# Kernel optimization log

Measured on AMD Instinct MI355X. Metric: run time of the kernel, lower is better.

## Reference

```python
import jax, jax.numpy as jnp
import numpy as np

# Tsit5 Butcher tableau (Tsitouras 2011), same coefficients diffrax uses.
C2, C3, C4, C5, C6 = 0.161, 0.327, 0.9, 0.9800255409045097, 1.0
A21 = 0.161
A31, A32 = -0.008480655492356989, 0.335480655492357
A41, A42, A43 = 2.8971530571054935, -6.359448489975075, 4.3622954328695815
A51, A52, A53, A54 = 5.325864828439257, -11.748883564062828, 7.4955393428898365, -0.09249506636175525
A61, A62, A63, A64, A65 = 5.86145544294642, -12.92096931784711, 8.159367898576159, -0.071584973281401, -0.028269050394068383
B1, B2, B3, B4, B5, B6 = 0.09646076681806523, 0.01, 0.4798896504144996, 1.379008574103742, -3.290069515436081, 2.324710524099774

DIM, WIDTH, DEPTH = 64, 256, 3
BATCH, NT = 4096, 101


def setup_inputs() -> dict:
    key = jax.random.key(0)
    ks = jax.random.split(key, 10)
    ts = jnp.linspace(0.0, 1.0, NT, dtype=jnp.float32)
    y0 = jax.random.normal(ks[0], (BATCH, DIM), dtype=jnp.float32)
    def lin(k, fan_in, fan_out):
        lim = 1.0 / np.sqrt(fan_in)
        kw, kb = jax.random.split(k)
        W = jax.random.uniform(kw, (fan_in, fan_out), jnp.float32, -lim, lim)
        b = jax.random.uniform(kb, (fan_out,), jnp.float32, -lim, lim)
        return W, b
    W0, b0 = lin(ks[1], DIM, WIDTH)
    W1, b1 = lin(ks[2], WIDTH, WIDTH)
    W2, b2 = lin(ks[3], WIDTH, WIDTH)
    W3, b3 = lin(ks[4], WIDTH, DIM)
    return {"ts": ts, "y0": y0, "W0": W0, "b0": b0, "W1": W1, "b1": b1,
            "W2": W2, "b2": b2, "W3": W3, "b3": b3}


def _vf(y, W0, b0, W1, b1, W2, b2, W3, b3):
    # MLP vector field f(t, y) = MLP(y); tanh hidden activations, depth=3 hidden layers.
    h = jnp.tanh(y @ W0 + b0)
    h = jnp.tanh(h @ W1 + b1)
    h = jnp.tanh(h @ W2 + b2)
    return h @ W3 + b3


def reference(ts, y0, W0, b0, W1, b1, W2, b2, W3, b3):
    f = lambda y: _vf(y, W0, b0, W1, b1, W2, b2, W3, b3)

    def tsit5_step(y, h):
        # h: scalar step size (broadcasts over [batch, dim])
        k1 = f(y)
        k2 = f(y + h * (A21 * k1))
        k3 = f(y + h * (A31 * k1 + A32 * k2))
        k4 = f(y + h * (A41 * k1 + A42 * k2 + A43 * k3))
        k5 = f(y + h * (A51 * k1 + A52 * k2 + A53 * k3 + A54 * k4))
        k6 = f(y + h * (A61 * k1 + A62 * k2 + A63 * k3 + A64 * k4 + A65 * k5))
        return y + h * (B1 * k1 + B2 * k2 + B3 * k3 + B4 * k4 + B5 * k5 + B6 * k6)

    def scan_body(y, hpair):
        y_new = tsit5_step(y, hpair)
        return y_new, y_new

    hs = ts[1:] - ts[:-1]                     # [NT-1] step sizes between save points
    hs = hs[:, None, None]                    # broadcast to [NT-1, 1, 1]
    _, ys_tail = jax.lax.scan(scan_body, y0, hs)
    return jnp.concatenate([y0[None], ys_tail], axis=0)  # [NT, batch, dim]
```

## Files before the change

kernel.cpp:

```cpp
#include <hip/hip_runtime.h>

#define NTIME   101
#define BATCH   4096
#define DIM     64
#define WIDTH   256
#define TB      16
#define NTHREADS 1024
#define AST     264
#define SPS     68

#define A21 0.161f
#define A31 (-0.008480655492356989f)
#define A32 0.335480655492357f
#define A41 2.8971530571054935f
#define A42 (-6.359448489975075f)
#define A43 4.3622954328695815f
#define A51 5.325864828439257f
#define A52 (-11.748883564062828f)
#define A53 7.4955393428898365f
#define A54 (-0.09249506636175525f)
#define A61 5.86145544294642f
#define A62 (-12.92096931784711f)
#define A63 8.159367898576159f
#define A64 (-0.071584973281401f)
#define A65 (-0.028269050394068383f)
#define B1 0.09646076681806523f
#define B2 0.01f
#define B3 0.4798896504144996f
#define B4 1.379008574103742f
#define B5 (-3.290069515436081f)
#define B6 2.324710524099774f

typedef float  floatx4 __attribute__((ext_vector_type(4)));
typedef _Float16 halfx8 __attribute__((ext_vector_type(8)));

#define L0S1 0
#define L0S2 16384
#define L1S1 32768
#define L1S2 98304
#define L2S1 163840
#define L2S2 229376
#define L3S1 294912
#define L3S2 311296

__device__ __forceinline__ float fast_tanh(float x) {
    float e = __expf(2.0f * x);
    return 1.0f - 2.0f / (e + 1.0f);
}

__device__ __forceinline__ void bar_lds() {
    asm volatile("s_waitcnt lgkmcnt(0)\n\ts_barrier" ::: "memory");
}

__global__ void pack_weights(const float* __restrict__ W0, const float* __restrict__ W1,
                             const float* __restrict__ W2, const float* __restrict__ W3,
                             _Float16* __restrict__ ws)
{
    int idx = blockIdx.x * 256 + threadIdx.x;
    const float* W; int K, N, e; size_t d1, d2;
    if (idx < 16384)       { W = W0; K = 64;  N = 256; e = idx;          d1 = L0S1; d2 = L0S2; }
    else if (idx < 81920)  { W = W1; K = 256; N = 256; e = idx - 16384;  d1 = L1S1; d2 = L1S2; }
    else if (idx < 147456) { W = W2; K = 256; N = 256; e = idx - 81920;  d1 = L2S1; d2 = L2S2; }
    else if (idx < 163840) { W = W3; K = 256; N = 64;  e = idx - 147456; d1 = L3S1; d2 = L3S2; }
    else return;
    int k = e / N, n = e % N;
    float w = W[e];
    _Float16 h1 = (_Float16)w;
    _Float16 h2 = (_Float16)((w - (float)h1) * 4096.0f);
    int kc = k >> 5, q = (k >> 3) & 3, j = k & 7, nt = n >> 4, nc = n & 15;
    size_t off = ((size_t)((nt * (K / 32) + kc) * 64 + q * 16 + nc)) * 8 + j;
    ws[d1 + off] = h1;
    ws[d2 + off] = h2;
}

template<int KCNT>
__device__ __forceinline__ void mfma_run(const _Float16* __restrict__ pA1,
                                         const _Float16* __restrict__ pA2,
                                         const _Float16* __restrict__ B1g,
                                         const _Float16* __restrict__ B2g,
                                         int fbBase, int kcStart, int lane,
                                         floatx4& acc1o, floatx4& acc2o)
{
    const int m = lane & 15, q = lane >> 4;
    floatx4 acc1 = (floatx4)0.0f, acc2 = (floatx4)0.0f;
    halfx8 va1[2], va2[2], vb1[2], vb2[2];

    const int aOff0 = m * AST + kcStart * 32 + q * 8;
    const size_t fOff0 = ((size_t)fbBase * 64 + lane) * 8;
    vb1[0] = *(const halfx8*)(B1g + fOff0);
    vb2[0] = *(const halfx8*)(B2g + fOff0);
    va1[0] = *(const halfx8*)(pA1 + aOff0);
    va2[0] = *(const halfx8*)(pA2 + aOff0);

    #pragma unroll
    for (int i = 0; i < KCNT; ++i) {
        const int cur = i & 1, nxt = cur ^ 1;
        if (i + 1 < KCNT) {
            const size_t fOff = ((size_t)(fbBase + i + 1) * 64 + lane) * 8;
            vb1[nxt] = *(const halfx8*)(B1g + fOff);
            vb2[nxt] = *(const halfx8*)(B2g + fOff);
            const int aOff = m * AST + (kcStart + i + 1) * 32 + q * 8;
            va1[nxt] = *(const halfx8*)(pA1 + aOff);
            va2[nxt] = *(const halfx8*)(pA2 + aOff);
        }
        acc1 = __builtin_amdgcn_mfma_f32_16x16x32_f16(va1[cur], vb1[cur], acc1, 0, 0, 0);
        acc2 = __builtin_amdgcn_mfma_f32_16x16x32_f16(va1[cur], vb2[cur], acc2, 0, 0, 0);
        acc2 = __builtin_amdgcn_mfma_f32_16x16x32_f16(va2[cur], vb1[cur], acc2, 0, 0, 0);
    }
    acc1o = acc1; acc2o = acc2;
}

__device__ __forceinline__ void hidden_epi(floatx4 a1, floatx4 a2,
                                           const float* __restrict__ bias,
                                           _Float16* __restrict__ o1,
                                           _Float16* __restrict__ o2,
                                           int w, int lane)
{
    const int m = lane & 15, q = lane >> 4;
    const int col = (w << 4) + m;
    const float bb = bias[col];
    #pragma unroll
    for (int v = 0; v < 4; ++v) {
        float val = fast_tanh(a1[v] + a2[v] * (1.0f / 4096.0f) + bb);
        _Float16 h1 = (_Float16)val;
        _Float16 h2 = (_Float16)((val - (float)h1) * 4096.0f);
        const int idx = (q * 4 + v) * AST + col;
        o1[idx] = h1;
        o2[idx] = h2;
    }
}

__global__ void __launch_bounds__(NTHREADS)
ode_kernel(const float* __restrict__ ts, const float* __restrict__ y0,
           const float* __restrict__ b0, const float* __restrict__ b1,
           const float* __restrict__ b2, const float* __restrict__ b3,
           const _Float16* __restrict__ ws, float* __restrict__ out)
{
    __shared__ __align__(16) _Float16 sA1[2][TB * AST];
    __shared__ __align__(16) _Float16 sA2[2][TB * AST];
    __shared__ __align__(16) _Float16 cW0[32768];
    __shared__ __align__(16) float sK[5][TB * DIM];
    __shared__ __align__(16) float sY[TB * DIM];
    __shared__ __align__(16) float sP[4][TB * SPS];
    __shared__ __align__(16) float sBias[832];

    const int tid  = threadIdx.x;
    const int lane = tid & 63;
    const int w    = tid >> 6;
    const long base = (long)blockIdx.x * (TB * DIM);
    const int c = tid & 63;
    const int r = tid >> 6;

    #pragma unroll
    for (int i = 0; i < 4; ++i)
        ((halfx8*)cW0)[tid + i * NTHREADS] = ((const halfx8*)(ws + L0S1))[tid + i * NTHREADS];

    if (tid < 832) {
        float v;
        if (tid < 256)      v = b0[tid];
        else if (tid < 512) v = b1[tid - 256];
        else if (tid < 768) v = b2[tid - 512];
        else                v = b3[tid - 768];
        sBias[tid] = v;
    }
    {
        float v = y0[base + tid];
        sY[tid] = v;
        __builtin_nontemporal_store(v, &out[base + tid]);
        _Float16 h1 = (_Float16)v;
        _Float16 h2 = (_Float16)((v - (float)h1) * 4096.0f);
        sA1[0][r * AST + c] = h1;
        sA2[0][r * AST + c] = h2;
    }
    __syncthreads();

    const int r68 = r * SPS + c;

    for (int t = 0; t < NTIME - 1; ++t) {
        const float h = ts[t + 1] - ts[t];

        #pragma unroll 1
        for (int s = 0; s < 6; ++s) {
            floatx4 a1, a2;
            mfma_run<2>(sA1[0], sA2[0], cW0, cW0 + 16384, w * 2, 0, lane, a1, a2);
            hidden_epi(a1, a2, sBias + 0, sA1[1], sA2[1], w, lane);
            bar_lds();
            mfma_run<8>(sA1[1], sA2[1], ws + L1S1, ws + L1S2, w * 8, 0, lane, a1, a2);
            hidden_epi(a1, a2, sBias + 256, sA1[0], sA2[0], w, lane);
            bar_lds();
            mfma_run<8>(sA1[0], sA2[0], ws + L2S1, ws + L2S2, w * 8, 0, lane, a1, a2);
            hidden_epi(a1, a2, sBias + 512, sA1[1], sA2[1], w, lane);
            bar_lds();
            {
                const int nt = w & 3, kg = w >> 2;
                mfma_run<2>(sA1[1], sA2[1], ws + L3S1, ws + L3S2,
                            nt * 8 + kg * 2, kg * 2, lane, a1, a2);
                const int m = lane & 15, q = lane >> 4;
                #pragma unroll
                for (int v = 0; v < 4; ++v)
                    sP[kg][(q * 4 + v) * SPS + nt * 16 + m]
                        = a1[v] + a2[v] * (1.0f / 4096.0f);
            }
            bar_lds();

            float kv = sP[0][r68] + sP[1][r68] + sP[2][r68] + sP[3][r68]
                     + sBias[768 + c];
            float v;
            if (s == 0) {
                sK[0][tid] = kv;
                v = fmaf(h, A21 * kv, sY[tid]);
            } else if (s == 1) {
                sK[1][tid] = kv;
                v = fmaf(h, fmaf(A31, sK[0][tid], A32 * kv), sY[tid]);
            } else if (s == 2) {
                sK[2][tid] = kv;
                float sum = A41 * sK[0][tid] + A42 * sK[1][tid] + A43 * kv;
                v = fmaf(h, sum, sY[tid]);
            } else if (s == 3) {
                sK[3][tid] = kv;
                float sum = A51 * sK[0][tid] + A52 * sK[1][tid] + A53 * sK[2][tid] + A54 * kv;
                v = fmaf(h, sum, sY[tid]);
            } else if (s == 4) {
                sK[4][tid] = kv;
                float sum = A61 * sK[0][tid] + A62 * sK[1][tid] + A63 * sK[2][tid]
                          + A64 * sK[3][tid] + A65 * kv;
                v = fmaf(h, sum, sY[tid]);
            } else {
                float sum = B1 * sK[0][tid] + B2 * sK[1][tid] + B3 * sK[2][tid]
                          + B4 * sK[3][tid] + B5 * sK[4][tid] + B6 * kv;
                v = fmaf(h, sum, sY[tid]);
                sY[tid] = v;
                __builtin_nontemporal_store(v, &out[(long)(t + 1) * (BATCH * DIM) + base + tid]);
            }
            _Float16 h1 = (_Float16)v;
            _Float16 h2 = (_Float16)((v - (float)h1) * 4096.0f);
            sA1[0][r * AST + c] = h1;
            sA2[0][r * AST + c] = h2;
            bar_lds();
        }
    }
}

extern "C" void kernel_launch(void* const* d_in, const int* in_sizes, int n_in,
                              void* d_out, int out_size, void* d_ws, size_t ws_size,
                              hipStream_t stream) {
    (void)in_sizes; (void)n_in; (void)ws_size; (void)out_size;
    const float* ts = (const float*)d_in[0];
    const float* y0 = (const float*)d_in[1];
    const float* W0 = (const float*)d_in[2];
    const float* b0 = (const float*)d_in[3];
    const float* W1 = (const float*)d_in[4];
    const float* b1 = (const float*)d_in[5];
    const float* W2 = (const float*)d_in[6];
    const float* b2 = (const float*)d_in[7];
    const float* W3 = (const float*)d_in[8];
    const float* b3 = (const float*)d_in[9];
    _Float16* ws = (_Float16*)d_ws;
    float* out = (float*)d_out;

    hipLaunchKernelGGL(pack_weights, dim3(640), dim3(256), 0, stream, W0, W1, W2, W3, ws);
    hipLaunchKernelGGL(ode_kernel, dim3(BATCH / TB), dim3(NTHREADS), 0, stream,
                       ts, y0, b0, b1, b2, b3, ws, out);
}
```

Measured before the change: 4.315 ms.

## XOR-swizzle activation LDS layout and prefetch next layer's first weight fragment

Applies an XOR swizzle to the column index of the fp16 activation tiles in shared memory, on both the write side (epilogue and state update) and the MFMA A-fragment reads, to reduce LDS bank conflicts. It also issues the global loads for the first B fragment of the next layer before the tanh epilogue and barrier, so that weight-load latency overlaps the epilogue. The swizzle must stay consistent across every writer and reader of the tiles, and the prefetch adds register pressure.

```diff
diff --git a/kernel.cpp b/kernel.cpp
--- a/kernel.cpp
+++ b/kernel.cpp
@@ -73,6 +73,52 @@
     ws[d2 + off] = h2;
 }
 
+
+__device__ __forceinline__ void load_b(const _Float16* __restrict__ g1,
+                                       const _Float16* __restrict__ g2,
+                                       int fb, int lane, halfx8& o1, halfx8& o2) {
+    const size_t f = ((size_t)fb * 64 + lane) * 8;
+    o1 = *(const halfx8*)(g1 + f);
+    o2 = *(const halfx8*)(g2 + f);
+}
+
+template<int KCNT>
+__device__ __forceinline__ void mfma_run_pre(const _Float16* __restrict__ pA1,
+                                             const _Float16* __restrict__ pA2,
+                                             const _Float16* __restrict__ B1g,
+                                             const _Float16* __restrict__ B2g,
+                                             int fbBase, int kcStart, int lane,
+                                             halfx8 pb1, halfx8 pb2,
+                                             floatx4& acc1o, floatx4& acc2o)
+{
+    const int m = lane & 15, q = lane >> 4;
+    const int qs = (q ^ ((m >> 2) & 3)) * 8;
+    floatx4 acc1 = (floatx4)0.0f, acc2 = (floatx4)0.0f;
+    halfx8 va1[2], va2[2], vb1[2], vb2[2];
+    vb1[0] = pb1; vb2[0] = pb2;
+
+    const int aOff0 = m * AST + kcStart * 32 + qs;
+    va1[0] = *(const halfx8*)(pA1 + aOff0);
+    va2[0] = *(const halfx8*)(pA2 + aOff0);
+
+    #pragma unroll
+    for (int i = 0; i < KCNT; ++i) {
+        const int cur = i & 1, nxt = cur ^ 1;
+        if (i + 1 < KCNT) {
+            const size_t fOff = ((size_t)(fbBase + i + 1) * 64 + lane) * 8;
+            vb1[nxt] = *(const halfx8*)(B1g + fOff);
+            vb2[nxt] = *(const halfx8*)(B2g + fOff);
+            const int aOff = m * AST + (kcStart + i + 1) * 32 + qs;
+            va1[nxt] = *(const halfx8*)(pA1 + aOff);
+            va2[nxt] = *(const halfx8*)(pA2 + aOff);
+        }
+        acc1 = __builtin_amdgcn_mfma_f32_16x16x32_f16(va1[cur], vb1[cur], acc1, 0, 0, 0);
+        acc2 = __builtin_amdgcn_mfma_f32_16x16x32_f16(va1[cur], vb2[cur], acc2, 0, 0, 0);
+        acc2 = __builtin_amdgcn_mfma_f32_16x16x32_f16(va2[cur], vb1[cur], acc2, 0, 0, 0);
+    }
+    acc1o = acc1; acc2o = acc2;
+}
+
 template<int KCNT>
 __device__ __forceinline__ void mfma_run(const _Float16* __restrict__ pA1,
                                          const _Float16* __restrict__ pA2,
@@ -82,10 +128,11 @@
                                          floatx4& acc1o, floatx4& acc2o)
 {
     const int m = lane & 15, q = lane >> 4;
+    const int qs = (q ^ ((m >> 2) & 3)) * 8;
     floatx4 acc1 = (floatx4)0.0f, acc2 = (floatx4)0.0f;
     halfx8 va1[2], va2[2], vb1[2], vb2[2];
 
-    const int aOff0 = m * AST + kcStart * 32 + q * 8;
+    const int aOff0 = m * AST + kcStart * 32 + qs;
     const size_t fOff0 = ((size_t)fbBase * 64 + lane) * 8;
     vb1[0] = *(const halfx8*)(B1g + fOff0);
     vb2[0] = *(const halfx8*)(B2g + fOff0);
@@ -99,7 +146,7 @@
             const size_t fOff = ((size_t)(fbBase + i + 1) * 64 + lane) * 8;
             vb1[nxt] = *(const halfx8*)(B1g + fOff);
             vb2[nxt] = *(const halfx8*)(B2g + fOff);
-            const int aOff = m * AST + (kcStart + i + 1) * 32 + q * 8;
+            const int aOff = m * AST + (kcStart + i + 1) * 32 + qs;
             va1[nxt] = *(const halfx8*)(pA1 + aOff);
             va2[nxt] = *(const halfx8*)(pA2 + aOff);
         }
@@ -118,13 +165,14 @@
 {
     const int m = lane & 15, q = lane >> 4;
     const int col = (w << 4) + m;
+    const int colS = col ^ (q << 3);
     const float bb = bias[col];
     #pragma unroll
     for (int v = 0; v < 4; ++v) {
         float val = fast_tanh(a1[v] + a2[v] * (1.0f / 4096.0f) + bb);
         _Float16 h1 = (_Float16)val;
         _Float16 h2 = (_Float16)((val - (float)h1) * 4096.0f);
-        const int idx = (q * 4 + v) * AST + col;
+        const int idx = (q * 4 + v) * AST + colS;
         o1[idx] = h1;
         o2[idx] = h2;
     }
@@ -150,6 +198,8 @@
     const long base = (long)blockIdx.x * (TB * DIM);
     const int c = tid & 63;
     const int r = tid >> 6;
+    const int nt = w & 3, kg = w >> 2;
+    const int cS = c ^ (((r >> 2) & 3) << 3);
 
     #pragma unroll
     for (int i = 0; i < 4; ++i)
@@ -169,8 +219,8 @@
         __builtin_nontemporal_store(v, &out[base + tid]);
         _Float16 h1 = (_Float16)v;
         _Float16 h2 = (_Float16)((v - (float)h1) * 4096.0f);
-        sA1[0][r * AST + c] = h1;
-        sA2[0][r * AST + c] = h2;
+        sA1[0][r * AST + cS] = h1;
+        sA2[0][r * AST + cS] = h2;
     }
     __syncthreads();
 
@@ -183,18 +233,25 @@
         for (int s = 0; s < 6; ++s) {
             floatx4 a1, a2;
             mfma_run<2>(sA1[0], sA2[0], cW0, cW0 + 16384, w * 2, 0, lane, a1, a2);
+            halfx8 pb1a, pb1b;
+            load_b(ws + L1S1, ws + L1S2, w * 8, lane, pb1a, pb1b);
             hidden_epi(a1, a2, sBias + 0, sA1[1], sA2[1], w, lane);
             bar_lds();
-            mfma_run<8>(sA1[1], sA2[1], ws + L1S1, ws + L1S2, w * 8, 0, lane, a1, a2);
+            mfma_run_pre<8>(sA1[1], sA2[1], ws + L1S1, ws + L1S2, w * 8, 0, lane,
+                            pb1a, pb1b, a1, a2);
+            halfx8 pb2a, pb2b;
+            load_b(ws + L2S1, ws + L2S2, w * 8, lane, pb2a, pb2b);
             hidden_epi(a1, a2, sBias + 256, sA1[0], sA2[0], w, lane);
             bar_lds();
-            mfma_run<8>(sA1[0], sA2[0], ws + L2S1, ws + L2S2, w * 8, 0, lane, a1, a2);
+            mfma_run_pre<8>(sA1[0], sA2[0], ws + L2S1, ws + L2S2, w * 8, 0, lane,
+                            pb2a, pb2b, a1, a2);
+            halfx8 pb3a, pb3b;
+            load_b(ws + L3S1, ws + L3S2, nt * 8 + kg * 2, lane, pb3a, pb3b);
             hidden_epi(a1, a2, sBias + 512, sA1[1], sA2[1], w, lane);
             bar_lds();
             {
-                const int nt = w & 3, kg = w >> 2;
-                mfma_run<2>(sA1[1], sA2[1], ws + L3S1, ws + L3S2,
-                            nt * 8 + kg * 2, kg * 2, lane, a1, a2);
+                mfma_run_pre<2>(sA1[1], sA2[1], ws + L3S1, ws + L3S2,
+                                nt * 8 + kg * 2, kg * 2, lane, pb3a, pb3b, a1, a2);
                 const int m = lane & 15, q = lane >> 4;
                 #pragma unroll
                 for (int v = 0; v < 4; ++v)
@@ -234,8 +291,8 @@
             }
             _Float16 h1 = (_Float16)v;
             _Float16 h2 = (_Float16)((v - (float)h1) * 4096.0f);
-            sA1[0][r * AST + c] = h1;
-            sA2[0][r * AST + c] = h2;
+            sA1[0][r * AST + cS] = h1;
+            sA2[0][r * AST + cS] = h2;
             bar_lds();
         }
     }
```

Measured after the change: 4.070 ms. -5.7%, faster.
